# Optimization experiments

Measured on AMD Instinct MI355X. Metric: run time of the kernel, lower is better.

## Reference

```python
import jax, jax.numpy as jnp
import numpy as np

N, D, E = 10000, 64, 32768   # nodes, padded degree, target edges
F, H, O = 64, 256, 1         # in_channels, hidden_channels, out_channels


def _linear_init(key, fin, fout):
    kw, kb = jax.random.split(key)
    s = 1.0 / np.sqrt(fin)
    w = jax.random.uniform(kw, (fin, fout), jnp.float32, -s, s)
    b = jax.random.uniform(kb, (fout,), jnp.float32, -s, s)
    return w, b


def setup_inputs() -> dict:
    key = jax.random.key(0)
    ks = jax.random.split(key, 12)
    x = jax.random.normal(ks[0], (N, F), jnp.float32)
    adj_nbr = jax.random.randint(ks[1], (N, D), 0, N)          # padded neighbor lists
    tar_ei = jax.random.randint(ks[2], (2, E), 0, N)           # target edges
    xcn_w1, xcn_b1 = _linear_init(ks[3], F, H)
    xcn_w2, xcn_b2 = _linear_init(ks[4], H, H)
    xcn_w3, xcn_b3 = _linear_init(ks[5], H, H)
    xij_w1, xij_b1 = _linear_init(ks[6], F, H)
    xij_w2, xij_b2 = _linear_init(ks[7], H, H)
    lin_w1, lin_b1 = _linear_init(ks[8], H, H)
    lin_w2, lin_b2 = _linear_init(ks[9], H, O)
    beta = jnp.ones((1,), jnp.float32)
    return dict(x=x, adj_nbr=adj_nbr, tar_ei=tar_ei, beta=beta,
                xcn_w1=xcn_w1, xcn_b1=xcn_b1, xcn_w2=xcn_w2, xcn_b2=xcn_b2,
                xcn_w3=xcn_w3, xcn_b3=xcn_b3,
                xij_w1=xij_w1, xij_b1=xij_b1, xij_w2=xij_w2, xij_b2=xij_b2,
                lin_w1=lin_w1, lin_b1=lin_b1, lin_w2=lin_w2, lin_b2=lin_b2)


def reference(x, adj_nbr, tar_ei, beta,
              xcn_w1, xcn_b1, xcn_w2, xcn_b2, xcn_w3, xcn_b3,
              xij_w1, xij_b1, xij_w2, xij_b2,
              lin_w1, lin_b1, lin_w2, lin_b2):
    relu = jax.nn.relu
    i, j = tar_ei[0], tar_ei[1]
    # adjoverlap: common-neighbor intersection of rows i and j of the adjacency
    ni = adj_nbr[i]                                   # [E, D] neighbors of i
    nj = adj_nbr[j]                                   # [E, D] neighbors of j
    cm = (ni[:, :, None] == nj[:, None, :]).any(-1)   # [E, D] ni[a] in N(j)?
    # spmm_add(cn, x): sum features of common neighbors per target edge
    xcn = jnp.einsum('ed,edf->ef', cm.astype(x.dtype), x[ni])  # [E, F]
    # xijlin(xi * xj): Linear -> ReLU -> Linear
    xij = x[i] * x[j]
    h_ij = relu(xij @ xij_w1 + xij_b1) @ xij_w2 + xij_b2
    # xcnlin(xcn): Linear -> ReLU -> Linear -> ReLU -> Linear
    h_cn = relu(xcn @ xcn_w1 + xcn_b1)
    h_cn = relu(h_cn @ xcn_w2 + xcn_b2)
    h_cn = h_cn @ xcn_w3 + xcn_b3
    # lin(xcnlin(xcn) * beta + xij): Linear -> ReLU -> Linear
    h = relu((h_cn * beta + h_ij) @ lin_w1 + lin_b1)
    return h @ lin_w2 + lin_b2                        # [E, O]
```

## Files before the change

### kernel.cpp

```cpp
#include <hip/hip_runtime.h>

#define NNODES 10000
#define DDEG   64
#define NEDGES 32768
#define FIN    64
#define HID    256

typedef __attribute__((ext_vector_type(8))) __bf16 bf16x8;
typedef __attribute__((ext_vector_type(4))) float  f32x4;

__device__ __forceinline__ unsigned short f2bf(float f) {
    unsigned x = __float_as_uint(f);
    return (unsigned short)((x + 0x7FFFu + ((x >> 16) & 1u)) >> 16);
}
__device__ __forceinline__ float b2f(unsigned short u) {
    return __uint_as_float(((unsigned)u) << 16);
}

#define OFF_XIJ1 0
#define OFF_XIJ2 16384
#define OFF_XCN1 81920
#define OFF_XCN2 98304
#define OFF_XCN3 163840
#define OFF_LIN1 229376
#define WT_TOTAL 294912
#define NTILES   36

__host__ __device__ constexpr int tile_off(int t) {
    return t < 2  ? OFF_XIJ1 + t * 8192
         : t < 10 ? OFF_XIJ2 + (t - 2) * 8192
         : t < 12 ? OFF_XCN1 + (t - 10) * 8192
         : t < 20 ? OFF_XCN2 + (t - 12) * 8192
         : t < 28 ? OFF_XCN3 + (t - 20) * 8192
         :          OFF_LIN1 + (t - 28) * 8192;
}

__device__ __forceinline__ void gll16(const unsigned short* g, unsigned short* l) {
    __builtin_amdgcn_global_load_lds(
        (const __attribute__((address_space(1))) unsigned int*)g,
        (__attribute__((address_space(3))) unsigned int*)l, 16, 0, 0);
}
__device__ __forceinline__ void stage_slice(const unsigned short* src, unsigned short* dst,
                                            int lane) {
#pragma unroll
    for (int c = 0; c < 4; ++c)
        gll16(src + c * 512 + lane * 8, dst + c * 512);
}
__device__ __forceinline__ void stage_act(const unsigned short* g, unsigned short* l,
                                          int tid, int wv) {
#pragma unroll
    for (int c = 0; c < 2; ++c)
        gll16(g + c * 2048 + tid * 8, l + c * 2048 + wv * 512);
}

__global__ __launch_bounds__(256) void edge_prep_k(const float* __restrict__ x,
                                                   const int* __restrict__ adj,
                                                   const int* __restrict__ tar,
                                                   const float* __restrict__ xij_w1,
                                                   const float* __restrict__ xij_w2,
                                                   const float* __restrict__ xcn_w1,
                                                   const float* __restrict__ xcn_w2,
                                                   const float* __restrict__ xcn_w3,
                                                   const float* __restrict__ lin_w1,
                                                   unsigned short* __restrict__ WT,
                                                   unsigned short* __restrict__ xij_g,
                                                   unsigned short* __restrict__ xcn_g) {
    const int wv   = threadIdx.x >> 6;
    const int lane = threadIdx.x & 63;
    const int e    = blockIdx.x * 4 + wv;

    int i = tar[e];
    int j = tar[NEDGES + e];
    int ni = adj[i * DDEG + lane];
    int nj = adj[j * DDEG + lane];
    float xi = x[i * FIN + lane];
    float xj = x[j * FIN + lane];

    bool found = false;
#pragma unroll
    for (int b = 0; b < 64; ++b)
        found |= (ni == (int)__builtin_amdgcn_readlane(nj, b));
    unsigned long long m = __ballot(found);

    float acc = 0.f;
    while (m) {
        int a = __ffsll(m) - 1;
        m &= m - 1;
        int r = (int)__builtin_amdgcn_readlane(ni, a);
        acc += x[r * FIN + lane];
    }
    int sl = lane ^ ((e & 7) << 3);
    xij_g[(size_t)e * FIN + sl] = f2bf(xi * xj);
    xcn_g[(size_t)e * FIN + sl] = f2bf(acc);

    if (blockIdx.x < WT_TOTAL / 256) {
        int idx = blockIdx.x * 256 + threadIdx.x;
        const float* src;
        int r;
        if (idx < OFF_XIJ2)      { r = idx - OFF_XIJ1; src = xij_w1; }
        else if (idx < OFF_XCN1) { r = idx - OFF_XIJ2; src = xij_w2; }
        else if (idx < OFF_XCN2) { r = idx - OFF_XCN1; src = xcn_w1; }
        else if (idx < OFF_XCN3) { r = idx - OFF_XCN2; src = xcn_w2; }
        else if (idx < OFF_LIN1) { r = idx - OFF_XCN3; src = xcn_w3; }
        else                     { r = idx - OFF_LIN1; src = lin_w1; }
        int kb  = r >> 13;
        int n   = (r & 8191) >> 5;
        int klo = r & 31;
        WT[idx] = f2bf(src[(kb * 32 + klo) * HID + n]);
    }
}

template <int T0, int NT, int LDA>
__device__ __forceinline__ void run_phase(const unsigned short* As,
                                          unsigned short* myring,
                                          const unsigned short* __restrict__ WT,
                                          int myslice, int lr, int lg, int lane,
                                          f32x4 acc[4][4]) {
#pragma unroll
    for (int m = 0; m < 4; ++m)
#pragma unroll
        for (int n = 0; n < 4; ++n) acc[m][n] = (f32x4){0.f, 0.f, 0.f, 0.f};
    const int sw = (lr & 7) << 3;
#pragma unroll
    for (int s = 0; s < NT; ++s) {
        const int t = T0 + s;
        if (t + 1 < NTILES)
            stage_slice(WT + tile_off(t + 1) + myslice, myring + ((t + 1) & 1) * 2048, lane);
        if (t + 1 < NTILES)
            asm volatile("s_waitcnt vmcnt(4)" ::: "memory");
        else
            asm volatile("s_waitcnt vmcnt(0)" ::: "memory");
        const unsigned short* cur = myring + (t & 1) * 2048;
        bf16x8 a[4], b[4];
#pragma unroll
        for (int n = 0; n < 4; ++n)
            b[n] = *reinterpret_cast<const bf16x8*>(&cur[(n * 16 + lr) * 32 + 8 * lg]);
#pragma unroll
        for (int m = 0; m < 4; ++m)
            a[m] = *reinterpret_cast<const bf16x8*>(
                &As[(m * 16 + lr) * LDA + ((s * 32 + 8 * lg) ^ sw)]);
        __builtin_amdgcn_s_setprio(1);
#pragma unroll
        for (int m = 0; m < 4; ++m)
#pragma unroll
            for (int n = 0; n < 4; ++n)
                acc[m][n] = __builtin_amdgcn_mfma_f32_16x16x32_bf16(a[m], b[n], acc[m][n], 0, 0, 0);
        __builtin_amdgcn_s_setprio(0);
    }
}

__device__ __forceinline__ void fence_barrier() {
    asm volatile("s_waitcnt lgkmcnt(0)" ::: "memory");
    __builtin_amdgcn_s_barrier();
}

__global__ __launch_bounds__(256) void mlp_k(const unsigned short* __restrict__ xij_g,
                                             const unsigned short* __restrict__ xcn_g,
                                             const unsigned short* __restrict__ WT,
                                             const float* __restrict__ xij_b1,
                                             const float* __restrict__ xij_b2,
                                             const float* __restrict__ xcn_b1,
                                             const float* __restrict__ xcn_b2,
                                             const float* __restrict__ xcn_b3,
                                             const float* __restrict__ lin_b1,
                                             const float* __restrict__ lin_w2,
                                             const float* __restrict__ lin_b2,
                                             const float* __restrict__ beta,
                                             float* __restrict__ out) {
    __shared__ unsigned short sX[64 * 64];
    __shared__ unsigned short sH[64 * 256];
    __shared__ unsigned short sBr[4 * 2 * 2048];

    const int tid  = threadIdx.x;
    const int wv   = tid >> 6;
    const int lane = tid & 63;
    const int lr   = lane & 15;
    const int lg   = lane >> 4;
    const int col0 = wv * 64;
    const int row0 = blockIdx.x * 64;
    const int myslice = wv * 2048;
    unsigned short* myring = sBr + wv * 4096;

    stage_act(xij_g + (size_t)row0 * FIN, sX, tid, wv);
    stage_slice(WT + tile_off(0) + myslice, myring, lane);
    const float betaf = beta[0];
    asm volatile("s_waitcnt vmcnt(4)" ::: "memory");
    __builtin_amdgcn_s_barrier();

    f32x4 acc[4][4];
    float bl[4];

    run_phase<0, 2, 64>(sX, myring, WT, myslice, lr, lg, lane, acc);
#pragma unroll
    for (int n = 0; n < 4; ++n) bl[n] = xij_b1[col0 + n * 16 + lr];
#pragma unroll
    for (int m = 0; m < 4; ++m)
#pragma unroll
        for (int n = 0; n < 4; ++n)
#pragma unroll
            for (int i = 0; i < 4; ++i) {
                int row = m * 16 + 4 * lg + i;
                int col = col0 + n * 16 + lr;
                sH[row * HID + (col ^ ((row & 7) << 3))] = f2bf(fmaxf(acc[m][n][i] + bl[n], 0.f));
            }
    fence_barrier();
    stage_act(xcn_g + (size_t)row0 * FIN, sX, tid, wv);

    run_phase<2, 8, 256>(sH, myring, WT, myslice, lr, lg, lane, acc);
#pragma unroll
    for (int n = 0; n < 4; ++n) bl[n] = xij_b2[col0 + n * 16 + lr];
    unsigned hij_lo[4][4], hij_hi[4][4];
#pragma unroll
    for (int m = 0; m < 4; ++m)
#pragma unroll
        for (int n = 0; n < 4; ++n) {
            hij_lo[m][n] = ((unsigned)f2bf(acc[m][n][1] + bl[n]) << 16) | f2bf(acc[m][n][0] + bl[n]);
            hij_hi[m][n] = ((unsigned)f2bf(acc[m][n][3] + bl[n]) << 16) | f2bf(acc[m][n][2] + bl[n]);
        }
    fence_barrier();

    run_phase<10, 2, 64>(sX, myring, WT, myslice, lr, lg, lane, acc);
#pragma unroll
    for (int n = 0; n < 4; ++n) bl[n] = xcn_b1[col0 + n * 16 + lr];
#pragma unroll
    for (int m = 0; m < 4; ++m)
#pragma unroll
        for (int n = 0; n < 4; ++n)
#pragma unroll
            for (int i = 0; i < 4; ++i) {
                int row = m * 16 + 4 * lg + i;
                int col = col0 + n * 16 + lr;
                sH[row * HID + (col ^ ((row & 7) << 3))] = f2bf(fmaxf(acc[m][n][i] + bl[n], 0.f));
            }
    fence_barrier();

    run_phase<12, 8, 256>(sH, myring, WT, myslice, lr, lg, lane, acc);
    fence_barrier();
#pragma unroll
    for (int n = 0; n < 4; ++n) bl[n] = xcn_b2[col0 + n * 16 + lr];
#pragma unroll
    for (int m = 0; m < 4; ++m)
#pragma unroll
        for (int n = 0; n < 4; ++n)
#pragma unroll
            for (int i = 0; i < 4; ++i) {
                int row = m * 16 + 4 * lg + i;
                int col = col0 + n * 16 + lr;
                sH[row * HID + (col ^ ((row & 7) << 3))] = f2bf(fmaxf(acc[m][n][i] + bl[n], 0.f));
            }
    fence_barrier();

    run_phase<20, 8, 256>(sH, myring, WT, myslice, lr, lg, lane, acc);
    fence_barrier();
#pragma unroll
    for (int n = 0; n < 4; ++n) bl[n] = xcn_b3[col0 + n * 16 + lr];
#pragma unroll
    for (int m = 0; m < 4; ++m)
#pragma unroll
        for (int n = 0; n < 4; ++n) {
            float h0 = b2f((unsigned short)(hij_lo[m][n] & 0xFFFF));
            float h1 = b2f((unsigned short)(hij_lo[m][n] >> 16));
            float h2 = b2f((unsigned short)(hij_hi[m][n] & 0xFFFF));
            float h3 = b2f((unsigned short)(hij_hi[m][n] >> 16));
            float v0 = (acc[m][n][0] + bl[n]) * betaf + h0;
            float v1 = (acc[m][n][1] + bl[n]) * betaf + h1;
            float v2 = (acc[m][n][2] + bl[n]) * betaf + h2;
            float v3 = (acc[m][n][3] + bl[n]) * betaf + h3;
            int rb = m * 16 + 4 * lg;
            int col = col0 + n * 16 + lr;
            sH[(rb + 0) * HID + (col ^ (((rb + 0) & 7) << 3))] = f2bf(v0);
            sH[(rb + 1) * HID + (col ^ (((rb + 1) & 7) << 3))] = f2bf(v1);
            sH[(rb + 2) * HID + (col ^ (((rb + 2) & 7) << 3))] = f2bf(v2);
            sH[(rb + 3) * HID + (col ^ (((rb + 3) & 7) << 3))] = f2bf(v3);
        }
    fence_barrier();

    run_phase<28, 8, 256>(sH, myring, WT, myslice, lr, lg, lane, acc);
#pragma unroll
    for (int n = 0; n < 4; ++n) bl[n] = lin_b1[col0 + n * 16 + lr];
    float w2l[4];
#pragma unroll
    for (int n = 0; n < 4; ++n) w2l[n] = lin_w2[col0 + n * 16 + lr];
    float* sRed = (float*)sX;
#pragma unroll
    for (int m = 0; m < 4; ++m) {
        float p[4] = {0.f, 0.f, 0.f, 0.f};
#pragma unroll
        for (int n = 0; n < 4; ++n)
#pragma unroll
            for (int i = 0; i < 4; ++i)
                p[i] += fmaxf(acc[m][n][i] + bl[n], 0.f) * w2l[n];
#pragma unroll
        for (int i = 0; i < 4; ++i) {
            float s = p[i];
            s += __shfl_xor(s, 1);
            s += __shfl_xor(s, 2);
            s += __shfl_xor(s, 4);
            s += __shfl_xor(s, 8);
            if (lr == 0) sRed[wv * 64 + m * 16 + 4 * lg + i] = s;
        }
    }
    __syncthreads();
    if (tid < 64)
        out[row0 + tid] = sRed[tid] + sRed[64 + tid] + sRed[128 + tid] + sRed[192 + tid] + lin_b2[0];
}

extern "C" void kernel_launch(void* const* d_in, const int* in_sizes, int n_in,
                              void* d_out, int out_size, void* d_ws, size_t ws_size,
                              hipStream_t stream) {
    const float* x      = (const float*)d_in[0];
    const int*   adj    = (const int*)d_in[1];
    const int*   tar    = (const int*)d_in[2];
    const float* beta   = (const float*)d_in[3];
    const float* xcn_w1 = (const float*)d_in[4];
    const float* xcn_b1 = (const float*)d_in[5];
    const float* xcn_w2 = (const float*)d_in[6];
    const float* xcn_b2 = (const float*)d_in[7];
    const float* xcn_w3 = (const float*)d_in[8];
    const float* xcn_b3 = (const float*)d_in[9];
    const float* xij_w1 = (const float*)d_in[10];
    const float* xij_b1 = (const float*)d_in[11];
    const float* xij_w2 = (const float*)d_in[12];
    const float* xij_b2 = (const float*)d_in[13];
    const float* lin_w1 = (const float*)d_in[14];
    const float* lin_b1 = (const float*)d_in[15];
    const float* lin_w2 = (const float*)d_in[16];
    const float* lin_b2 = (const float*)d_in[17];

    unsigned short* WT    = (unsigned short*)d_ws;
    unsigned short* xij_g = (unsigned short*)((char*)d_ws + 589824);
    unsigned short* xcn_g = (unsigned short*)((char*)d_ws + 4784128);

    edge_prep_k<<<NEDGES / 4, 256, 0, stream>>>(x, adj, tar,
                                                xij_w1, xij_w2, xcn_w1, xcn_w2, xcn_w3, lin_w1,
                                                WT, xij_g, xcn_g);
    mlp_k<<<NEDGES / 64, 256, 0, stream>>>(xij_g, xcn_g, WT,
                                           xij_b1, xij_b2, xcn_b1, xcn_b2, xcn_b3,
                                           lin_b1, lin_w2, lin_b2, beta, (float*)d_out);
}
```

Baseline: 70.05 us.

## Load weight tiles directly into registers and spill h_ij to global scratch

Weight B-fragments are no longer staged through a per-wave LDS ring. They are loaded straight from global memory into a 4-deep register queue, prefetched four tiles ahead, and the ring's shared memory is freed. The h_ij intermediate moves from registers to a global scratch buffer and is read back later, and both activation inputs are staged up front. Together with __launch_bounds__(256,2), this aims to cut LDS use and register pressure so two blocks fit per CU. In exchange it adds global round-trips for h_ij and relies on cache hits for the direct weight loads.

```diff
diff --git a/kernel.cpp b/kernel.cpp
--- a/kernel.cpp
+++ b/kernel.cpp
@@ -39,12 +39,6 @@
     __builtin_amdgcn_global_load_lds(
         (const __attribute__((address_space(1))) unsigned int*)g,
         (__attribute__((address_space(3))) unsigned int*)l, 16, 0, 0);
-}
-__device__ __forceinline__ void stage_slice(const unsigned short* src, unsigned short* dst,
-                                            int lane) {
-#pragma unroll
-    for (int c = 0; c < 4; ++c)
-        gll16(src + c * 512 + lane * 8, dst + c * 512);
 }
 __device__ __forceinline__ void stage_act(const unsigned short* g, unsigned short* l,
                                           int tid, int wv) {
@@ -112,10 +106,9 @@
 
 template <int T0, int NT, int LDA>
 __device__ __forceinline__ void run_phase(const unsigned short* As,
-                                          unsigned short* myring,
                                           const unsigned short* __restrict__ WT,
-                                          int myslice, int lr, int lg, int lane,
-                                          f32x4 acc[4][4]) {
+                                          int boff, int lr, int lg,
+                                          bf16x8 (&bq)[4][4], f32x4 acc[4][4]) {
 #pragma unroll
     for (int m = 0; m < 4; ++m)
 #pragma unroll
@@ -124,17 +117,7 @@
 #pragma unroll
     for (int s = 0; s < NT; ++s) {
         const int t = T0 + s;
-        if (t + 1 < NTILES)
-            stage_slice(WT + tile_off(t + 1) + myslice, myring + ((t + 1) & 1) * 2048, lane);
-        if (t + 1 < NTILES)
-            asm volatile("s_waitcnt vmcnt(4)" ::: "memory");
-        else
-            asm volatile("s_waitcnt vmcnt(0)" ::: "memory");
-        const unsigned short* cur = myring + (t & 1) * 2048;
-        bf16x8 a[4], b[4];
-#pragma unroll
-        for (int n = 0; n < 4; ++n)
-            b[n] = *reinterpret_cast<const bf16x8*>(&cur[(n * 16 + lr) * 32 + 8 * lg]);
+        bf16x8 a[4];
 #pragma unroll
         for (int m = 0; m < 4; ++m)
             a[m] = *reinterpret_cast<const bf16x8*>(
@@ -144,8 +127,14 @@
         for (int m = 0; m < 4; ++m)
 #pragma unroll
             for (int n = 0; n < 4; ++n)
-                acc[m][n] = __builtin_amdgcn_mfma_f32_16x16x32_bf16(a[m], b[n], acc[m][n], 0, 0, 0);
+                acc[m][n] = __builtin_amdgcn_mfma_f32_16x16x32_bf16(a[m], bq[t & 3][n], acc[m][n], 0, 0, 0);
         __builtin_amdgcn_s_setprio(0);
+        if (t + 4 < NTILES) {
+#pragma unroll
+            for (int n = 0; n < 4; ++n)
+                bq[(t + 4) & 3][n] = *reinterpret_cast<const bf16x8*>(
+                    &WT[tile_off(t + 4) + boff + n * 512]);
+        }
     }
 }
 
@@ -154,22 +143,23 @@
     __builtin_amdgcn_s_barrier();
 }
 
-__global__ __launch_bounds__(256) void mlp_k(const unsigned short* __restrict__ xij_g,
-                                             const unsigned short* __restrict__ xcn_g,
-                                             const unsigned short* __restrict__ WT,
-                                             const float* __restrict__ xij_b1,
-                                             const float* __restrict__ xij_b2,
-                                             const float* __restrict__ xcn_b1,
-                                             const float* __restrict__ xcn_b2,
-                                             const float* __restrict__ xcn_b3,
-                                             const float* __restrict__ lin_b1,
-                                             const float* __restrict__ lin_w2,
-                                             const float* __restrict__ lin_b2,
-                                             const float* __restrict__ beta,
-                                             float* __restrict__ out) {
-    __shared__ unsigned short sX[64 * 64];
+__global__ __launch_bounds__(256, 2) void mlp_k(const unsigned short* __restrict__ xij_g,
+                                                const unsigned short* __restrict__ xcn_g,
+                                                const unsigned short* __restrict__ WT,
+                                                unsigned* __restrict__ hij_g,
+                                                const float* __restrict__ xij_b1,
+                                                const float* __restrict__ xij_b2,
+                                                const float* __restrict__ xcn_b1,
+                                                const float* __restrict__ xcn_b2,
+                                                const float* __restrict__ xcn_b3,
+                                                const float* __restrict__ lin_b1,
+                                                const float* __restrict__ lin_w2,
+                                                const float* __restrict__ lin_b2,
+                                                const float* __restrict__ beta,
+                                                float* __restrict__ out) {
+    __shared__ unsigned short sXij[64 * 64];
+    __shared__ unsigned short sXcn[64 * 64];
     __shared__ unsigned short sH[64 * 256];
-    __shared__ unsigned short sBr[4 * 2 * 2048];
 
     const int tid  = threadIdx.x;
     const int wv   = tid >> 6;
@@ -178,19 +168,25 @@
     const int lg   = lane >> 4;
     const int col0 = wv * 64;
     const int row0 = blockIdx.x * 64;
-    const int myslice = wv * 2048;
-    unsigned short* myring = sBr + wv * 4096;
-
-    stage_act(xij_g + (size_t)row0 * FIN, sX, tid, wv);
-    stage_slice(WT + tile_off(0) + myslice, myring, lane);
+    const int boff = (col0 + lr) * 32 + 8 * lg;
+
+    stage_act(xij_g + (size_t)row0 * FIN, sXij, tid, wv);
+    stage_act(xcn_g + (size_t)row0 * FIN, sXcn, tid, wv);
+    bf16x8 bq[4][4];
+#pragma unroll
+    for (int t = 0; t < 4; ++t)
+#pragma unroll
+        for (int n = 0; n < 4; ++n)
+            bq[t][n] = *reinterpret_cast<const bf16x8*>(&WT[tile_off(t) + boff + n * 512]);
     const float betaf = beta[0];
-    asm volatile("s_waitcnt vmcnt(4)" ::: "memory");
+    unsigned* hbase = hij_g + (size_t)(blockIdx.x * 4 + wv) * 2048 + lane * 2;
+    asm volatile("s_waitcnt vmcnt(16)" ::: "memory");
     __builtin_amdgcn_s_barrier();
 
     f32x4 acc[4][4];
     float bl[4];
 
-    run_phase<0, 2, 64>(sX, myring, WT, myslice, lr, lg, lane, acc);
+    run_phase<0, 2, 64>(sXij, WT, boff, lr, lg, bq, acc);
 #pragma unroll
     for (int n = 0; n < 4; ++n) bl[n] = xij_b1[col0 + n * 16 + lr];
 #pragma unroll
@@ -204,22 +200,22 @@
                 sH[row * HID + (col ^ ((row & 7) << 3))] = f2bf(fmaxf(acc[m][n][i] + bl[n], 0.f));
             }
     fence_barrier();
-    stage_act(xcn_g + (size_t)row0 * FIN, sX, tid, wv);
-
-    run_phase<2, 8, 256>(sH, myring, WT, myslice, lr, lg, lane, acc);
+
+    run_phase<2, 8, 256>(sH, WT, boff, lr, lg, bq, acc);
 #pragma unroll
     for (int n = 0; n < 4; ++n) bl[n] = xij_b2[col0 + n * 16 + lr];
-    unsigned hij_lo[4][4], hij_hi[4][4];
 #pragma unroll
     for (int m = 0; m < 4; ++m)
 #pragma unroll
         for (int n = 0; n < 4; ++n) {
-            hij_lo[m][n] = ((unsigned)f2bf(acc[m][n][1] + bl[n]) << 16) | f2bf(acc[m][n][0] + bl[n]);
-            hij_hi[m][n] = ((unsigned)f2bf(acc[m][n][3] + bl[n]) << 16) | f2bf(acc[m][n][2] + bl[n]);
+            uint2 v;
+            v.x = ((unsigned)f2bf(acc[m][n][1] + bl[n]) << 16) | f2bf(acc[m][n][0] + bl[n]);
+            v.y = ((unsigned)f2bf(acc[m][n][3] + bl[n]) << 16) | f2bf(acc[m][n][2] + bl[n]);
+            *reinterpret_cast<uint2*>(hbase + (m * 4 + n) * 128) = v;
         }
     fence_barrier();
 
-    run_phase<10, 2, 64>(sX, myring, WT, myslice, lr, lg, lane, acc);
+    run_phase<10, 2, 64>(sXcn, WT, boff, lr, lg, bq, acc);
 #pragma unroll
     for (int n = 0; n < 4; ++n) bl[n] = xcn_b1[col0 + n * 16 + lr];
 #pragma unroll
@@ -234,7 +230,7 @@
             }
     fence_barrier();
 
-    run_phase<12, 8, 256>(sH, myring, WT, myslice, lr, lg, lane, acc);
+    run_phase<12, 8, 256>(sH, WT, boff, lr, lg, bq, acc);
     fence_barrier();
 #pragma unroll
     for (int n = 0; n < 4; ++n) bl[n] = xcn_b2[col0 + n * 16 + lr];
@@ -250,7 +246,7 @@
             }
     fence_barrier();
 
-    run_phase<20, 8, 256>(sH, myring, WT, myslice, lr, lg, lane, acc);
+    run_phase<20, 8, 256>(sH, WT, boff, lr, lg, bq, acc);
     fence_barrier();
 #pragma unroll
     for (int n = 0; n < 4; ++n) bl[n] = xcn_b3[col0 + n * 16 + lr];
@@ -258,10 +254,11 @@
     for (int m = 0; m < 4; ++m)
 #pragma unroll
         for (int n = 0; n < 4; ++n) {
-            float h0 = b2f((unsigned short)(hij_lo[m][n] & 0xFFFF));
-            float h1 = b2f((unsigned short)(hij_lo[m][n] >> 16));
-            float h2 = b2f((unsigned short)(hij_hi[m][n] & 0xFFFF));
-            float h3 = b2f((unsigned short)(hij_hi[m][n] >> 16));
+            uint2 v = *reinterpret_cast<const uint2*>(hbase + (m * 4 + n) * 128);
+            float h0 = b2f((unsigned short)(v.x & 0xFFFF));
+            float h1 = b2f((unsigned short)(v.x >> 16));
+            float h2 = b2f((unsigned short)(v.y & 0xFFFF));
+            float h3 = b2f((unsigned short)(v.y >> 16));
             float v0 = (acc[m][n][0] + bl[n]) * betaf + h0;
             float v1 = (acc[m][n][1] + bl[n]) * betaf + h1;
             float v2 = (acc[m][n][2] + bl[n]) * betaf + h2;
@@ -275,13 +272,13 @@
         }
     fence_barrier();
 
-    run_phase<28, 8, 256>(sH, myring, WT, myslice, lr, lg, lane, acc);
+    run_phase<28, 8, 256>(sH, WT, boff, lr, lg, bq, acc);
 #pragma unroll
     for (int n = 0; n < 4; ++n) bl[n] = lin_b1[col0 + n * 16 + lr];
     float w2l[4];
 #pragma unroll
     for (int n = 0; n < 4; ++n) w2l[n] = lin_w2[col0 + n * 16 + lr];
-    float* sRed = (float*)sX;
+    float* sRed = (float*)sXij;
 #pragma unroll
     for (int m = 0; m < 4; ++m) {
         float p[4] = {0.f, 0.f, 0.f, 0.f};
@@ -330,11 +327,12 @@
     unsigned short* WT    = (unsigned short*)d_ws;
     unsigned short* xij_g = (unsigned short*)((char*)d_ws + 589824);
     unsigned short* xcn_g = (unsigned short*)((char*)d_ws + 4784128);
+    unsigned*       hij_g = (unsigned*)((char*)d_ws + 8978432);
 
     edge_prep_k<<<NEDGES / 4, 256, 0, stream>>>(x, adj, tar,
                                                 xij_w1, xij_w2, xcn_w1, xcn_w2, xcn_w3, lin_w1,
                                                 WT, xij_g, xcn_g);
-    mlp_k<<<NEDGES / 64, 256, 0, stream>>>(xij_g, xcn_g, WT,
+    mlp_k<<<NEDGES / 64, 256, 0, stream>>>(xij_g, xcn_g, WT, hij_g,
                                            xij_b1, xij_b2, xcn_b1, xcn_b2, xcn_b3,
                                            lin_b1, lin_w2, lin_b2, beta, (float*)d_out);
 }
```

Result: faster. 58.34 us, median of 2 (-16.7%).
